# Kernel optimization log

Hardware: AMD Instinct MI355X
Metric: run time of the kernel (lower is better)

## Reference

```python
import jax, jax.numpy as jnp
import numpy as np

D = 16          # input_dim (no augmentations)
HID = 256       # hidden_dim
WIN = 64        # window_size
LEN = 1000      # len_noise
INTU = 50       # len_interval_u
B = 512
PAIRS = D * (D - 1) // 2      # 120 depth-2 Lyndon pairs
LOGSIG = D + PAIRS            # 136 logsignature channels


def _static_schedule():
    """Replicates compute_multilevel_logsignature's index logic on static times."""
    tb = np.linspace(0.0, 1.0, LEN)
    tu = tb[::INTU]
    tt = np.linspace(0.0, 1.0, WIN)
    u_indices = np.searchsorted(tb, tu, side='right') - 1
    t_indices = np.searchsorted(tb, tt[1:], side='right') - 1
    u_idx_for_t = np.searchsorted(tu, tt[1:], side='right') - 1
    start_idx = u_indices[np.maximum(u_idx_for_t, 0)]
    # build u_logsigrnn times and the per-step last_h update mask
    qt, last = [], -1
    for iu in u_idx_for_t:
        iu = max(int(iu), 0)
        if iu != last:
            qt.append(tu[iu]); last = iu
    qt.append(tt[-1])
    upd = np.zeros(WIN, dtype=bool)
    for i, t in enumerate(tt):
        if qt and t >= qt[0]:
            qt.pop(0); upd[i] = True
    return tb, t_indices, start_idx, upd


def setup_inputs() -> dict:
    key = jax.random.key(0)
    ks = jax.random.split(key, 6)
    def lin(k, fo, fi):  # kaiming-style fan_in init
        return jax.random.normal(k, (fo, fi), jnp.float32) * np.float32(np.sqrt(2.0 / fi))
    return {
        "z": jax.random.normal(ks[0], (B, LEN, D), jnp.float32),
        "W1": lin(ks[1], HID, HID + LOGSIG), "b1": jnp.zeros((HID,), jnp.float32),
        "W2": lin(ks[2], HID, HID),          "b2": jnp.zeros((HID,), jnp.float32),
        "W3": lin(ks[3], HID, HID),          "b3": jnp.zeros((HID,), jnp.float32),
        "W_lin": lin(ks[4], HID, HID),
    }


def reference(z, W1, b1, W2, b2, W3, b3, W_lin):
    tb, t_idx, s_idx, upd = _static_schedule()
    # Brownian path: z[:,0]=0, z[:,1:] *= sqrt(dt), cumsum
    dt_sqrt = jnp.sqrt(jnp.asarray(np.diff(tb), jnp.float32))          # [LEN-1]
    z = jnp.concatenate([jnp.zeros_like(z[:, :1]), z[:, 1:] * dt_sqrt[None, :, None]], axis=1)
    X = jnp.cumsum(z, axis=1)                                           # [B,LEN,D]
    # depth-2 logsignature with basepoint=0: level1 = X[end]; level2 = Levy area
    iu, ju = np.triu_indices(D, 1)
    Xp, dX = X[:, :-1], X[:, 1:] - X[:, :-1]
    pair = Xp[..., iu] * dX[..., ju] - Xp[..., ju] * dX[..., iu]        # [B,LEN-1,PAIRS]
    C = jnp.concatenate([jnp.zeros_like(pair[:, :1]), jnp.cumsum(pair, axis=1)], axis=1)
    lvl1 = X[:, t_idx]
    levy = 0.5 * (C[:, t_idx] - C[:, s_idx])
    logsig = jnp.concatenate([lvl1, levy], axis=-1)
    logsig = jnp.concatenate([jnp.zeros_like(logsig[:, :1]), logsig], axis=1)  # prepend zeros
    seq = jnp.moveaxis(logsig, 1, 0)

    def mlp(v):  # FeedForwardNN([hid,hid]) + Tanh
        v = jax.nn.relu(v @ W1.T + b1)
        v = jax.nn.relu(v @ W2.T + b2)
        return jnp.tanh(v @ W3.T + b3)

    def step(last_h, xs):
        ls, u = xs
        h = mlp(jnp.concatenate([last_h, ls], axis=-1))
        new_last = jnp.where(u, h, last_h)
        return new_last, h @ W_lin.T

    h0 = jnp.zeros((z.shape[0], HID), z.dtype)  # init_fixed=True
    _, ys = jax.lax.scan(step, h0, (seq, jnp.asarray(upd)))
    return jnp.moveaxis(ys, 0, 1)
```

## Files before the change

### kernel.cpp

```cpp
#include <hip/hip_runtime.h>
#include <hip/hip_bf16.h>
#include <cmath>
#include <cstring>

#define B_SZ   512
#define SLEN   1000
#define DD     16
#define HID    256
#define WIN    64
#define PAIRS  120
#define LSIG   136
#define NWIN   20
#define MAXST  21
#define K1P    416
#define W1FN   (13 * 16 * 64 * 8)
#define WFN    (8 * 16 * 64 * 8)
#define PSTEP  21

using short8  = __attribute__((ext_vector_type(8))) short;
using short4v = __attribute__((ext_vector_type(4))) short;
using half8   = __attribute__((ext_vector_type(8))) _Float16;
using f32x4   = __attribute__((ext_vector_type(4))) float;

struct SchedArgs { short snapk[SLEN - 1]; };
struct CombPArgs { unsigned char winofm[WIN]; unsigned char zl[WIN]; unsigned char sstep[WIN]; };
struct ChainArgs { int nsteps; unsigned char kU[32]; };
struct FuseArgs  { unsigned char sidx[WIN]; };

__device__ __forceinline__ unsigned short f2h(float x) {
  _Float16 h = (_Float16)x;
  return __builtin_bit_cast(unsigned short, h);
}
__device__ __forceinline__ float ftanh(float x) {
  float t = fminf(fmaxf(2.f * x, -30.f), 30.f);
  float e = __expf(t);
  return (e - 1.f) / (e + 1.f);
}

__global__ __launch_bounds__(128) void prep_kernel(
    const float* __restrict__ z,
    const float* __restrict__ W1, const float* __restrict__ W2,
    const float* __restrict__ W3, const float* __restrict__ Wl,
    float* __restrict__ logsig, float* __restrict__ dxwin,
    unsigned short* __restrict__ W1f, unsigned short* __restrict__ W2f,
    unsigned short* __restrict__ W3f, unsigned short* __restrict__ Wlf,
    SchedArgs A)
{
  const int w = blockIdx.x, b = blockIdx.y, tid = threadIdx.x;
  if (w >= NWIN) {
    const int slot = ((w - NWIN) * B_SZ + b) * 128 + tid;
    for (int e = slot; e < W1FN + 3 * WFN; e += 3 * B_SZ * 128) {
      if (e < W1FN) {
        int f = e;
        int j = f & 7, l15 = (f >> 3) & 15, lq = (f >> 7) & 3, nsub = (f >> 9) & 15, kk = f >> 13;
        int row = nsub * 16 + l15, col = kk * 32 + lq * 8 + j;
        float v = (col < HID + LSIG) ? W1[(size_t)row * (HID + LSIG) + col] : 0.f;
        W1f[f] = f2h(v);
      } else {
        int e2 = e - W1FN;
        int which = e2 >> 16, f = e2 & 65535;
        int j = f & 7, l15 = (f >> 3) & 15, lq = (f >> 7) & 3, nsub = (f >> 9) & 15, kk = (f >> 13) & 7;
        int row = nsub * 16 + l15, col = kk * 32 + lq * 8 + j;
        const float* src = which == 0 ? W2 : which == 1 ? W3 : Wl;
        unsigned short* dst = which == 0 ? W2f : which == 1 ? W3f : Wlf;
        dst[f] = f2h(src[(size_t)row * HID + col]);
      }
    }
    return;
  }
  __shared__ float zs[50][16];
  const int ns = (w == NWIN - 1) ? 49 : 50;
  const float* src = z + ((size_t)b * SLEN + 50 * w + 1) * DD;
  const double s999 = 1.0 / (double)(SLEN - 1);
  for (int c = tid; c < ns * 4; c += 128) {
    float4 v = ((const float4*)src)[c];
    int t = 50 * w + (c >> 2);
    double a = (t + 1 == SLEN - 1) ? 1.0 : (double)(t + 1) * s999;
    float s = sqrtf((float)(a - (double)t * s999));
    v.x *= s; v.y *= s; v.z *= s; v.w *= s;
    ((float4*)&zs[0][0])[c] = v;
  }
  int pi = 0, pj = 0;
  if (tid < PAIRS) { int rem = tid, i = 0; while (rem >= DD - 1 - i) { rem -= DD - 1 - i; ++i; } pi = i; pj = i + 1 + rem; }
  __syncthreads();
  float Yi = 0.f, Yj = 0.f, LL = 0.f, Yd = 0.f;
  const int base_t = 50 * w;
  for (int u = 0; u < ns; ++u) {
    const float di = zs[u][pi], dj = zs[u][pj];
    LL = fmaf(Yi, dj, LL); LL = fmaf(-Yj, di, LL);
    Yi += di; Yj += dj;
    if (tid < DD) Yd += zs[u][tid];
    const int m = A.snapk[base_t + u];
    if (m) {
      float* dst = logsig + ((size_t)b * WIN + m) * LSIG;
      if (tid < DD)    dst[tid]      = Yd;
      if (tid < PAIRS) dst[DD + tid] = LL;
    }
  }
  if (tid < DD) dxwin[((size_t)b * NWIN + w) * DD + tid] = Yd;
}

__global__ __launch_bounds__(256) void combp_kernel(
    float* __restrict__ logsig, const float* __restrict__ dxwin,
    const unsigned short* __restrict__ W1f, const float* __restrict__ b1,
    float* __restrict__ partial, CombPArgs A)
{
  __shared__ float Xs[16][16], Yt[16][16];
  __shared__ __align__(16) unsigned short As[20 * 16 * 8];
  const int k = blockIdx.x, g = blockIdx.y, tid = threadIdx.x;
  const int w = A.winofm[k], zl = A.zl[k], ss = A.sstep[k];
  for (int c = tid; c < 3 * 16 * 8; c += 256) As[17 * 16 * 8 + c] = 0;
  {
    const int bi = tid >> 4, col = tid & 15;
    const size_t b = (size_t)(g * 16 + bi);
    float acc = 0.f;
    for (int ww = 0; ww < w; ++ww) acc += dxwin[(b * NWIN + ww) * DD + col];
    float y = (k == 0) ? 0.f : logsig[(b * WIN + k) * LSIG + col];
    float fin = (k == 0) ? 0.f : acc + y;
    Xs[bi][col] = acc; Yt[bi][col] = y;
    logsig[(b * WIN + k) * LSIG + col] = fin;
    As[((col >> 3) * 16 + bi) * 8 + (col & 7)] = f2h(fin);
  }
  __syncthreads();
  for (int idx = tid; idx < 16 * PAIRS; idx += 256) {
    const int bi = idx / PAIRS, p = idx - bi * PAIRS;
    int rem = p, i = 0; while (rem >= DD - 1 - i) { rem -= DD - 1 - i; ++i; }
    const int pi = i, pj = i + 1 + rem;
    const size_t b = (size_t)(g * 16 + bi);
    float ll = (k == 0) ? 0.f : logsig[(b * WIN + k) * LSIG + DD + p];
    float fin = (k == 0 || zl) ? 0.f
              : 0.5f * (ll + Xs[bi][pi] * Yt[bi][pj] - Xs[bi][pj] * Yt[bi][pi]);
    logsig[(b * WIN + k) * LSIG + DD + p] = fin;
    const int c = DD + p;
    As[((c >> 3) * 16 + bi) * 8 + (c & 7)] = f2h(fin);
  }
  if (ss == 255) return;
  __syncthreads();
  const int lane = tid & 63, wv = tid >> 6;
  const int l15 = lane & 15, lq = lane >> 4;
  f32x4 acc4[4] = {{0,0,0,0},{0,0,0,0},{0,0,0,0},{0,0,0,0}};
#pragma unroll
  for (int kt = 0; kt < 5; ++kt) {
    half8 af = *(const half8*)&As[((kt * 4 + lq) * 16 + l15) * 8];
#pragma unroll
    for (int t = 0; t < 4; ++t) {
      half8 bfW = *(const half8*)(W1f + ((size_t)((8 + kt) * 16 + wv * 4 + t) * 64 + lane) * 8);
      acc4[t] = __builtin_amdgcn_mfma_f32_16x16x32_f16(bfW, af, acc4[t], 0, 0, 0);
    }
  }
#pragma unroll
  for (int t = 0; t < 4; ++t) {
    const int col0 = wv * 64 + t * 16 + lq * 4;
    f32x4 bb = *(const f32x4*)(b1 + col0);
    f32x4 r = acc4[t] + bb;
    *(f32x4*)&partial[(((size_t)g * PSTEP + ss) * 16 + l15) * HID + col0] = r;
  }
}

__global__ __attribute__((amdgpu_flat_work_group_size(512, 512)))
__attribute__((amdgpu_waves_per_eu(2, 2)))
void chain_kernel(
    const float* __restrict__ partial,
    const unsigned short* __restrict__ W1f, const unsigned short* __restrict__ W2f,
    const unsigned short* __restrict__ W3f,
    const float* __restrict__ b2, const float* __restrict__ b3,
    unsigned short* __restrict__ statesb, ChainArgs A)
{
  __shared__ __align__(16) unsigned short A0s[32 * 16 * 8];
  __shared__ __align__(16) unsigned short A1s[32 * 16 * 8];
  __shared__ __align__(16) unsigned short A2s[32 * 16 * 8];
  const int tid = threadIdx.x, g = blockIdx.x;
  const int lane = tid & 63, w = tid >> 6;
  const int l15 = lane & 15, lq = lane >> 4;

  for (int c = tid; c < 32 * 16 * 8; c += 512) A0s[c] = 0;
  for (int c = tid; c < 16 * HID; c += 512) {
    int r = c >> 8, col = c & 255;
    statesb[((size_t)(g * 16 + r) * MAXST + 0) * HID + col] = 0;
  }

  half8 W1r[16], W2r[16], W3r[16];
#pragma unroll
  for (int kk = 0; kk < 8; ++kk)
#pragma unroll
    for (int nt = 0; nt < 2; ++nt) {
      W1r[kk * 2 + nt] = *(const half8*)(W1f + ((size_t)(kk * 16 + w * 2 + nt) * 64 + lane) * 8);
      W2r[kk * 2 + nt] = *(const half8*)(W2f + ((size_t)(kk * 16 + w * 2 + nt) * 64 + lane) * 8);
      W3r[kk * 2 + nt] = *(const half8*)(W3f + ((size_t)(kk * 16 + w * 2 + nt) * 64 + lane) * 8);
    }

  int colb[2];
  f32x4 bias2v[2], bias3v[2];
#pragma unroll
  for (int nt = 0; nt < 2; ++nt) {
    colb[nt] = w * 32 + nt * 16 + lq * 4;
    bias2v[nt] = *(const f32x4*)(b2 + colb[nt]);
    bias3v[nt] = *(const f32x4*)(b3 + colb[nt]);
  }

  const float* pbase = partial + (size_t)g * PSTEP * 16 * HID;
  int poff[2];
#pragma unroll
  for (int nt = 0; nt < 2; ++nt) poff[nt] = l15 * HID + colb[nt];
  f32x4 pf[2];
  pf[0] = *(const f32x4*)(pbase + poff[0]);
  pf[1] = *(const f32x4*)(pbase + poff[1]);

  short4v hv4[2];
  __syncthreads();

  for (int m = 0; m < A.nsteps; ++m) {
    if (m > 0) {
#pragma unroll
      for (int nt = 0; nt < 2; ++nt)
        *(short4v*)&statesb[((size_t)(g * 16 + l15) * MAXST + m) * HID + colb[nt]] = hv4[nt];
    }
    {
      f32x4 acc[2][2];
      acc[0][0] = pf[0]; acc[0][1] = pf[1];
      acc[1][0] = (f32x4){0.f,0.f,0.f,0.f}; acc[1][1] = (f32x4){0.f,0.f,0.f,0.f};
      if (m + 1 < A.nsteps) {
        const float* pp = pbase + (size_t)(m + 1) * 16 * HID;
        pf[0] = *(const f32x4*)(pp + poff[0]);
        pf[1] = *(const f32x4*)(pp + poff[1]);
      }
#pragma unroll
      for (int kk = 0; kk < 8; ++kk) {
        half8 af = *(const half8*)&A0s[((kk * 4 + lq) * 16 + l15) * 8];
        acc[kk & 1][0] = __builtin_amdgcn_mfma_f32_16x16x32_f16(W1r[kk * 2    ], af, acc[kk & 1][0], 0, 0, 0);
        acc[kk & 1][1] = __builtin_amdgcn_mfma_f32_16x16x32_f16(W1r[kk * 2 + 1], af, acc[kk & 1][1], 0, 0, 0);
      }
#pragma unroll
      for (int nt = 0; nt < 2; ++nt) {
        f32x4 s = acc[0][nt] + acc[1][nt];
        short4v h4;
#pragma unroll
        for (int r4 = 0; r4 < 4; ++r4) h4[r4] = (short)f2h(fmaxf(s[r4], 0.f));
        *(short4v*)&A1s[((colb[nt] >> 3) * 16 + l15) * 8 + (colb[nt] & 7)] = h4;
      }
    }
    __syncthreads();
    {
      f32x4 acc[2][2] = {{{0.f,0.f,0.f,0.f},{0.f,0.f,0.f,0.f}},{{0.f,0.f,0.f,0.f},{0.f,0.f,0.f,0.f}}};
#pragma unroll
      for (int kk = 0; kk < 8; ++kk) {
        half8 af = *(const half8*)&A1s[((kk * 4 + lq) * 16 + l15) * 8];
        acc[kk & 1][0] = __builtin_amdgcn_mfma_f32_16x16x32_f16(W2r[kk * 2    ], af, acc[kk & 1][0], 0, 0, 0);
        acc[kk & 1][1] = __builtin_amdgcn_mfma_f32_16x16x32_f16(W2r[kk * 2 + 1], af, acc[kk & 1][1], 0, 0, 0);
      }
#pragma unroll
      for (int nt = 0; nt < 2; ++nt) {
        f32x4 s = acc[0][nt] + acc[1][nt] + bias2v[nt];
        short4v h4;
#pragma unroll
        for (int r4 = 0; r4 < 4; ++r4) h4[r4] = (short)f2h(fmaxf(s[r4], 0.f));
        *(short4v*)&A2s[((colb[nt] >> 3) * 16 + l15) * 8 + (colb[nt] & 7)] = h4;
      }
    }
    __syncthreads();
    {
      f32x4 acc[2][2] = {{{0.f,0.f,0.f,0.f},{0.f,0.f,0.f,0.f}},{{0.f,0.f,0.f,0.f},{0.f,0.f,0.f,0.f}}};
#pragma unroll
      for (int kk = 0; kk < 8; ++kk) {
        half8 af = *(const half8*)&A2s[((kk * 4 + lq) * 16 + l15) * 8];
        acc[kk & 1][0] = __builtin_amdgcn_mfma_f32_16x16x32_f16(W3r[kk * 2    ], af, acc[kk & 1][0], 0, 0, 0);
        acc[kk & 1][1] = __builtin_amdgcn_mfma_f32_16x16x32_f16(W3r[kk * 2 + 1], af, acc[kk & 1][1], 0, 0, 0);
      }
#pragma unroll
      for (int nt = 0; nt < 2; ++nt) {
        f32x4 s = acc[0][nt] + acc[1][nt] + bias3v[nt];
        short4v h4;
#pragma unroll
        for (int r4 = 0; r4 < 4; ++r4) h4[r4] = (short)f2h(ftanh(s[r4]));
        hv4[nt] = h4;
        *(short4v*)&A0s[((colb[nt] >> 3) * 16 + l15) * 8 + (colb[nt] & 7)] = h4;
      }
    }
    __syncthreads();
  }
  {
    const int m = A.nsteps;
#pragma unroll
    for (int nt = 0; nt < 2; ++nt)
      *(short4v*)&statesb[((size_t)(g * 16 + l15) * MAXST + m) * HID + colb[nt]] = hv4[nt];
  }
}

__global__ __launch_bounds__(256, 1) void fused_kernel(
    const unsigned short* __restrict__ statesb, const float* __restrict__ logsig,
    const unsigned short* __restrict__ W1f, const unsigned short* __restrict__ W2f,
    const unsigned short* __restrict__ W3f, const unsigned short* __restrict__ Wlf,
    const float* __restrict__ b1, const float* __restrict__ b2, const float* __restrict__ b3,
    float* __restrict__ out, FuseArgs F)
{
  __shared__ __align__(16) unsigned short act1[32 * 128 * 8];
  __shared__ __align__(16) unsigned short act2[32 * 128 * 8];
  __shared__ __align__(16) unsigned short atile[2][4 * 128 * 8];
  const int tid = threadIdx.x, band = blockIdx.x;
  const int lane = tid & 63, w = tid >> 6;
  const int l15 = lane & 15, lq = lane >> 4;

  f32x4 acc[8][4];
#pragma unroll
  for (int a = 0; a < 8; ++a)
#pragma unroll
    for (int t = 0; t < 4; ++t) acc[a][t] = (f32x4){0.f, 0.f, 0.f, 0.f};

  short8 pk[2];
  auto loadA = [&](int kk, short8* p) {
#pragma unroll
    for (int i = 0; i < 2; ++i) {
      int c = tid + 256 * i;
      int r = c >> 2, cc = (c & 3) * 8;
      int col = kk * 32 + cc;
      int bA = band * 2 + (r >> 6), ks = r & 63;
      if (col < HID) {
        p[i] = *(const short8*)(statesb + ((size_t)bA * MAXST + F.sidx[ks]) * HID + col);
      } else {
        const float* sp = logsig + ((size_t)bA * WIN + ks) * LSIG + (col - HID);
        float4 v0 = ((const float4*)sp)[0];
        float4 v1 = ((const float4*)sp)[1];
        short8 q;
        q[0] = (short)f2h(v0.x); q[1] = (short)f2h(v0.y); q[2] = (short)f2h(v0.z); q[3] = (short)f2h(v0.w);
        q[4] = (short)f2h(v1.x); q[5] = (short)f2h(v1.y); q[6] = (short)f2h(v1.z); q[7] = (short)f2h(v1.w);
        p[i] = q;
      }
    }
  };
  loadA(0, pk);
  for (int kk = 0; kk < 13; ++kk) {
    unsigned short* buf = &atile[kk & 1][0];
#pragma unroll
    for (int i = 0; i < 2; ++i) {
      int c = tid + 256 * i;
      int r = c >> 2, ch = c & 3;
      *(short8*)&buf[(ch * 128 + r) * 8] = pk[i];
    }
    __syncthreads();
    if (kk + 1 < 13) loadA(kk + 1, pk);
    half8 bfr[4];
#pragma unroll
    for (int t = 0; t < 4; ++t)
      bfr[t] = *(const half8*)(W1f + ((size_t)(kk * 16 + w * 4 + t) * 64 + lane) * 8);
#pragma unroll
    for (int a = 0; a < 8; ++a) {
      half8 af = *(const half8*)&buf[(lq * 128 + a * 16 + l15) * 8];
#pragma unroll
      for (int t = 0; t < 4; ++t)
        acc[a][t] = __builtin_amdgcn_mfma_f32_16x16x32_f16(bfr[t], af, acc[a][t], 0, 0, 0);
    }
  }
#pragma unroll
  for (int t = 0; t < 4; ++t) {
    const int col0 = w * 64 + t * 16 + lq * 4;
    f32x4 bb = *(const f32x4*)(b1 + col0);
#pragma unroll
    for (int a = 0; a < 8; ++a) {
      const int row = a * 16 + l15;
      short4v h4;
#pragma unroll
      for (int r4 = 0; r4 < 4; ++r4) h4[r4] = (short)f2h(fmaxf(acc[a][t][r4] + bb[r4], 0.f));
      *(short4v*)&act1[((col0 >> 3) * 128 + row) * 8 + (col0 & 7)] = h4;
    }
  }
  __syncthreads();

  auto layer = [&](const unsigned short* inb, const unsigned short* Wf) {
#pragma unroll
    for (int a = 0; a < 8; ++a)
#pragma unroll
      for (int t = 0; t < 4; ++t) acc[a][t] = (f32x4){0.f, 0.f, 0.f, 0.f};
    for (int kk = 0; kk < 8; ++kk) {
      half8 bfr[4];
#pragma unroll
      for (int t = 0; t < 4; ++t)
        bfr[t] = *(const half8*)(Wf + ((size_t)(kk * 16 + w * 4 + t) * 64 + lane) * 8);
#pragma unroll
      for (int a = 0; a < 8; ++a) {
        half8 af = *(const half8*)&inb[((kk * 4 + lq) * 128 + a * 16 + l15) * 8];
#pragma unroll
        for (int t = 0; t < 4; ++t)
          acc[a][t] = __builtin_amdgcn_mfma_f32_16x16x32_f16(bfr[t], af, acc[a][t], 0, 0, 0);
      }
    }
  };

  layer(act1, W2f);
#pragma unroll
  for (int t = 0; t < 4; ++t) {
    const int col0 = w * 64 + t * 16 + lq * 4;
    f32x4 bb = *(const f32x4*)(b2 + col0);
#pragma unroll
    for (int a = 0; a < 8; ++a) {
      const int row = a * 16 + l15;
      short4v h4;
#pragma unroll
      for (int r4 = 0; r4 < 4; ++r4) h4[r4] = (short)f2h(fmaxf(acc[a][t][r4] + bb[r4], 0.f));
      *(short4v*)&act2[((col0 >> 3) * 128 + row) * 8 + (col0 & 7)] = h4;
    }
  }
  __syncthreads();

  layer(act2, W3f);
#pragma unroll
  for (int t = 0; t < 4; ++t) {
    const int col0 = w * 64 + t * 16 + lq * 4;
    f32x4 bb = *(const f32x4*)(b3 + col0);
#pragma unroll
    for (int a = 0; a < 8; ++a) {
      const int row = a * 16 + l15;
      short4v h4;
#pragma unroll
      for (int r4 = 0; r4 < 4; ++r4) h4[r4] = (short)f2h(ftanh(acc[a][t][r4] + bb[r4]));
      *(short4v*)&act1[((col0 >> 3) * 128 + row) * 8 + (col0 & 7)] = h4;
    }
  }
  __syncthreads();

  layer(act1, Wlf);
#pragma unroll
  for (int t = 0; t < 4; ++t) {
    const int col0 = w * 64 + t * 16 + lq * 4;
#pragma unroll
    for (int a = 0; a < 8; ++a) {
      const int row = a * 16 + l15;
      *(f32x4*)&out[((size_t)(band * 128 + row)) * HID + col0] = acc[a][t];
    }
  }
}

static void build_sched(SchedArgs& P, CombPArgs& CB, ChainArgs& CH, FuseArgs& FU) {
  double tb[SLEN], tt[WIN], tu[NWIN];
  const double s999 = 1.0 / (double)(SLEN - 1);
  const double s63  = 1.0 / (double)(WIN - 1);
  for (int i = 0; i < SLEN; ++i) tb[i] = (double)i * s999;
  tb[SLEN - 1] = 1.0;
  for (int k = 0; k < WIN; ++k) tt[k] = (double)k * s63;
  tt[WIN - 1] = 1.0;
  for (int j = 0; j < NWIN; ++j) tu[j] = tb[50 * j];

  int t_idx[WIN - 1], u_for_t[WIN - 1];
  for (int k = 1; k < WIN; ++k) {
    int ii = 0;
    for (int q = 0; q < SLEN; ++q) if (tb[q] <= tt[k]) ii = q;
    t_idx[k - 1] = ii;
    int jj = 0;
    for (int q = 0; q < NWIN; ++q) if (tu[q] <= tt[k]) jj = q;
    u_for_t[k - 1] = jj;
  }
  for (int t = 0; t < SLEN - 1; ++t) P.snapk[t] = 0;
  for (int m = 1; m < WIN; ++m) P.snapk[t_idx[m - 1] - 1] = (short)m;

  for (int m = 0; m < WIN; ++m) { CB.winofm[m] = 0; CB.zl[m] = 0; CB.sstep[m] = 255; }
  for (int m = 1; m < WIN; ++m) {
    int p = t_idx[m - 1];
    CB.winofm[m] = (unsigned char)((p - 1) / 50);
    CB.zl[m] = (p % 50 == 0) ? 1 : 0;
  }

  double qt[32]; int nq = 0, last = -1;
  for (int m = 0; m < WIN - 1; ++m) {
    const int iu = u_for_t[m];
    if (iu != last) { qt[nq++] = tu[iu]; last = iu; }
  }
  qt[nq++] = tt[WIN - 1];
  int upd[WIN]; int qh = 0;
  for (int i = 0; i < WIN; ++i) {
    upd[i] = 0;
    if (qh < nq && tt[i] >= qt[qh]) { qh++; upd[i] = 1; }
  }
  int nU = 0;
  for (int k = 0; k < WIN; ++k) if (upd[k]) { if (nU < 32) CH.kU[nU] = (unsigned char)k; ++nU; }
  int cnt = 0;
  for (int k = 0; k < WIN; ++k) { FU.sidx[k] = (unsigned char)cnt; if (upd[k]) ++cnt; }
  CH.nsteps = FU.sidx[WIN - 1];
  for (int s = 0; s < nU && s < 32; ++s)
    if (s < PSTEP) CB.sstep[CH.kU[s]] = (unsigned char)s;
}

extern "C" void kernel_launch(void* const* d_in, const int* in_sizes, int n_in,
                              void* d_out, int out_size, void* d_ws, size_t ws_size,
                              hipStream_t stream) {
  const float* z  = (const float*)d_in[0];
  const float* W1 = (const float*)d_in[1];
  const float* b1 = (const float*)d_in[2];
  const float* W2 = (const float*)d_in[3];
  const float* b2 = (const float*)d_in[4];
  const float* W3 = (const float*)d_in[5];
  const float* b3 = (const float*)d_in[6];
  const float* Wl = (const float*)d_in[7];

  char* ws = (char*)d_ws;
  float* logsig = (float*)(ws);
  size_t o = (size_t)B_SZ * WIN * LSIG * 4;
  float* dxwin            = (float*)(ws + o); o += (size_t)B_SZ * NWIN * DD * 4;
  unsigned short* statesb = (unsigned short*)(ws + o); o += (size_t)B_SZ * MAXST * HID * 2;
  unsigned short* W1f     = (unsigned short*)(ws + o); o += (size_t)W1FN * 2;
  unsigned short* W2f     = (unsigned short*)(ws + o); o += (size_t)WFN * 2;
  unsigned short* W3f     = (unsigned short*)(ws + o); o += (size_t)WFN * 2;
  unsigned short* Wlf     = (unsigned short*)(ws + o); o += (size_t)WFN * 2;
  float* partial          = (float*)(ws + o); o += (size_t)32 * PSTEP * 16 * HID * 4;

  SchedArgs P; CombPArgs CB; ChainArgs CH; FuseArgs FU;
  build_sched(P, CB, CH, FU);

  prep_kernel<<<dim3(NWIN + 3, B_SZ), 128, 0, stream>>>(
      z, W1, W2, W3, Wl, logsig, dxwin, W1f, W2f, W3f, Wlf, P);
  combp_kernel<<<dim3(WIN, 32), 256, 0, stream>>>(logsig, dxwin, W1f, b1, partial, CB);
  chain_kernel<<<32, 512, 0, stream>>>(partial, W1f, W2f, W3f, b2, b3, statesb, CH);
  fused_kernel<<<256, 256, 0, stream>>>(statesb, logsig, W1f, W2f, W3f, Wlf,
                                        b1, b2, b3, (float*)d_out, FU);
}
```

Before: 230.5 us.

## Split fused MLP kernel into 32-row tiles with more blocks per CU

```diff
diff --git a/kernel.cpp b/kernel.cpp
--- a/kernel.cpp
+++ b/kernel.cpp
@@ -286,65 +286,54 @@
   }
 }
 
-__global__ __launch_bounds__(256, 1) void fused_kernel(
+__global__ __launch_bounds__(256, 4) void fused_kernel(
     const unsigned short* __restrict__ statesb, const float* __restrict__ logsig,
     const unsigned short* __restrict__ W1f, const unsigned short* __restrict__ W2f,
     const unsigned short* __restrict__ W3f, const unsigned short* __restrict__ Wlf,
     const float* __restrict__ b1, const float* __restrict__ b2, const float* __restrict__ b3,
     float* __restrict__ out, FuseArgs F)
 {
-  __shared__ __align__(16) unsigned short act1[32 * 128 * 8];
-  __shared__ __align__(16) unsigned short act2[32 * 128 * 8];
-  __shared__ __align__(16) unsigned short atile[2][4 * 128 * 8];
-  const int tid = threadIdx.x, band = blockIdx.x;
+  __shared__ __align__(16) unsigned short act[32 * 32 * 8];
+  __shared__ __align__(16) unsigned short atile[2][4 * 32 * 8];
+  const int tid = threadIdx.x;
+  const int b = blockIdx.x >> 1, half = blockIdx.x & 1;
   const int lane = tid & 63, w = tid >> 6;
   const int l15 = lane & 15, lq = lane >> 4;
 
-  f32x4 acc[8][4];
-#pragma unroll
-  for (int a = 0; a < 8; ++a)
+  f32x4 acc[2][4];
+#pragma unroll
+  for (int a = 0; a < 2; ++a)
 #pragma unroll
     for (int t = 0; t < 4; ++t) acc[a][t] = (f32x4){0.f, 0.f, 0.f, 0.f};
 
-  short8 pk[2];
-  auto loadA = [&](int kk, short8* p) {
-#pragma unroll
-    for (int i = 0; i < 2; ++i) {
-      int c = tid + 256 * i;
-      int r = c >> 2, cc = (c & 3) * 8;
-      int col = kk * 32 + cc;
-      int bA = band * 2 + (r >> 6), ks = r & 63;
-      if (col < HID) {
-        p[i] = *(const short8*)(statesb + ((size_t)bA * MAXST + F.sidx[ks]) * HID + col);
-      } else {
-        const float* sp = logsig + ((size_t)bA * WIN + ks) * LSIG + (col - HID);
-        float4 v0 = ((const float4*)sp)[0];
-        float4 v1 = ((const float4*)sp)[1];
-        short8 q;
-        q[0] = (short)f2h(v0.x); q[1] = (short)f2h(v0.y); q[2] = (short)f2h(v0.z); q[3] = (short)f2h(v0.w);
-        q[4] = (short)f2h(v1.x); q[5] = (short)f2h(v1.y); q[6] = (short)f2h(v1.z); q[7] = (short)f2h(v1.w);
-        p[i] = q;
-      }
+  const int lr = tid >> 3, lcc = (tid & 7) * 4;
+  const int lks = half * 32 + lr;
+  short4v pk;
+  auto loadA = [&](int kk) {
+    int col = kk * 32 + lcc;
+    if (col < HID) {
+      pk = *(const short4v*)(statesb + ((size_t)b * MAXST + F.sidx[lks]) * HID + col);
+    } else {
+      const float* sp = logsig + ((size_t)b * WIN + lks) * LSIG + (col - HID);
+      float4 v = *(const float4*)sp;
+      short4v q;
+      q[0] = (short)f2h(v.x); q[1] = (short)f2h(v.y); q[2] = (short)f2h(v.z); q[3] = (short)f2h(v.w);
+      pk = q;
     }
   };
-  loadA(0, pk);
+  loadA(0);
   for (int kk = 0; kk < 13; ++kk) {
     unsigned short* buf = &atile[kk & 1][0];
-#pragma unroll
-    for (int i = 0; i < 2; ++i) {
-      int c = tid + 256 * i;
-      int r = c >> 2, ch = c & 3;
-      *(short8*)&buf[(ch * 128 + r) * 8] = pk[i];
-    }
+    *(short4v*)&buf[((lcc >> 3) * 32 + lr) * 8 + (lcc & 7)] = pk;
     __syncthreads();
-    if (kk + 1 < 13) loadA(kk + 1, pk);
+    if (kk + 1 < 13) loadA(kk + 1);
     half8 bfr[4];
 #pragma unroll
     for (int t = 0; t < 4; ++t)
       bfr[t] = *(const half8*)(W1f + ((size_t)(kk * 16 + w * 4 + t) * 64 + lane) * 8);
 #pragma unroll
-    for (int a = 0; a < 8; ++a) {
-      half8 af = *(const half8*)&buf[(lq * 128 + a * 16 + l15) * 8];
+    for (int a = 0; a < 2; ++a) {
+      half8 af = *(const half8*)&buf[(lq * 32 + a * 16 + l15) * 8];
 #pragma unroll
       for (int t = 0; t < 4; ++t)
         acc[a][t] = __builtin_amdgcn_mfma_f32_16x16x32_f16(bfr[t], af, acc[a][t], 0, 0, 0);
@@ -355,19 +344,19 @@
     const int col0 = w * 64 + t * 16 + lq * 4;
     f32x4 bb = *(const f32x4*)(b1 + col0);
 #pragma unroll
-    for (int a = 0; a < 8; ++a) {
+    for (int a = 0; a < 2; ++a) {
       const int row = a * 16 + l15;
       short4v h4;
 #pragma unroll
       for (int r4 = 0; r4 < 4; ++r4) h4[r4] = (short)f2h(fmaxf(acc[a][t][r4] + bb[r4], 0.f));
-      *(short4v*)&act1[((col0 >> 3) * 128 + row) * 8 + (col0 & 7)] = h4;
-    }
-  }
-  __syncthreads();
-
-  auto layer = [&](const unsigned short* inb, const unsigned short* Wf) {
-#pragma unroll
-    for (int a = 0; a < 8; ++a)
+      *(short4v*)&act[((col0 >> 3) * 32 + row) * 8 + (col0 & 7)] = h4;
+    }
+  }
+  __syncthreads();
+
+  auto layer = [&](const unsigned short* Wf) {
+#pragma unroll
+    for (int a = 0; a < 2; ++a)
 #pragma unroll
       for (int t = 0; t < 4; ++t) acc[a][t] = (f32x4){0.f, 0.f, 0.f, 0.f};
     for (int kk = 0; kk < 8; ++kk) {
@@ -376,8 +365,8 @@
       for (int t = 0; t < 4; ++t)
         bfr[t] = *(const half8*)(Wf + ((size_t)(kk * 16 + w * 4 + t) * 64 + lane) * 8);
 #pragma unroll
-      for (int a = 0; a < 8; ++a) {
-        half8 af = *(const half8*)&inb[((kk * 4 + lq) * 128 + a * 16 + l15) * 8];
+      for (int a = 0; a < 2; ++a) {
+        half8 af = *(const half8*)&act[((kk * 4 + lq) * 32 + a * 16 + l15) * 8];
 #pragma unroll
         for (int t = 0; t < 4; ++t)
           acc[a][t] = __builtin_amdgcn_mfma_f32_16x16x32_f16(bfr[t], af, acc[a][t], 0, 0, 0);
@@ -385,46 +374,48 @@
     }
   };
 
-  layer(act1, W2f);
+  layer(W2f);
+  __syncthreads();
 #pragma unroll
   for (int t = 0; t < 4; ++t) {
     const int col0 = w * 64 + t * 16 + lq * 4;
     f32x4 bb = *(const f32x4*)(b2 + col0);
 #pragma unroll
-    for (int a = 0; a < 8; ++a) {
+    for (int a = 0; a < 2; ++a) {
       const int row = a * 16 + l15;
       short4v h4;
 #pragma unroll
       for (int r4 = 0; r4 < 4; ++r4) h4[r4] = (short)f2h(fmaxf(acc[a][t][r4] + bb[r4], 0.f));
-      *(short4v*)&act2[((col0 >> 3) * 128 + row) * 8 + (col0 & 7)] = h4;
-    }
-  }
-  __syncthreads();
-
-  layer(act2, W3f);
+      *(short4v*)&act[((col0 >> 3) * 32 + row) * 8 + (col0 & 7)] = h4;
+    }
+  }
+  __syncthreads();
+
+  layer(W3f);
+  __syncthreads();
 #pragma unroll
   for (int t = 0; t < 4; ++t) {
     const int col0 = w * 64 + t * 16 + lq * 4;
     f32x4 bb = *(const f32x4*)(b3 + col0);
 #pragma unroll
-    for (int a = 0; a < 8; ++a) {
+    for (int a = 0; a < 2; ++a) {
       const int row = a * 16 + l15;
       short4v h4;
 #pragma unroll
       for (int r4 = 0; r4 < 4; ++r4) h4[r4] = (short)f2h(ftanh(acc[a][t][r4] + bb[r4]));
-      *(short4v*)&act1[((col0 >> 3) * 128 + row) * 8 + (col0 & 7)] = h4;
-    }
-  }
-  __syncthreads();
-
-  layer(act1, Wlf);
+      *(short4v*)&act[((col0 >> 3) * 32 + row) * 8 + (col0 & 7)] = h4;
+    }
+  }
+  __syncthreads();
+
+  layer(Wlf);
 #pragma unroll
   for (int t = 0; t < 4; ++t) {
     const int col0 = w * 64 + t * 16 + lq * 4;
 #pragma unroll
-    for (int a = 0; a < 8; ++a) {
-      const int row = a * 16 + l15;
-      *(f32x4*)&out[((size_t)(band * 128 + row)) * HID + col0] = acc[a][t];
+    for (int a = 0; a < 2; ++a) {
+      const int ks = half * 32 + a * 16 + l15;
+      *(f32x4*)&out[((size_t)b * WIN + ks) * HID + col0] = acc[a][t];
     }
   }
 }
@@ -508,6 +499,6 @@
       z, W1, W2, W3, Wl, logsig, dxwin, W1f, W2f, W3f, Wlf, P);
   combp_kernel<<<dim3(WIN, 32), 256, 0, stream>>>(logsig, dxwin, W1f, b1, partial, CB);
   chain_kernel<<<32, 512, 0, stream>>>(partial, W1f, W2f, W3f, b2, b3, statesb, CH);
-  fused_kernel<<<256, 256, 0, stream>>>(statesb, logsig, W1f, W2f, W3f, Wlf,
-                                        b1, b2, b3, (float*)d_out, FU);
-}
+  fused_kernel<<<1024, 256, 0, stream>>>(statesb, logsig, W1f, W2f, W3f, Wlf,
+                                         b1, b2, b3, (float*)d_out, FU);
+}
```

Result: faster. 218.0 us (-5.4%).
